# Optimization experiments

Hardware: AMD Instinct MI355X
Metric: run time of the kernel (lower is better)

The kernel has to match this reference:

```python
import jax, jax.numpy as jnp
import numpy as np

K = 64          # number of tags, incl. BOS/EOS
V = 50000       # vocab size (excl. BOS/EOS words)
D = 128         # lexicon embedding dim
BOS_T = K - 2   # BOS tag index
EOS_T = K - 1   # EOS tag index
BATCH = 8192
L = 126         # interior words per sentence (n = L + 2 incl. BOS/EOS)
EPS = 1e-45     # smoothing added to A and B in updateAB


def setup_inputs() -> dict:
    key = jax.random.key(0)
    k1, k2, k3, k4 = jax.random.split(key, 4)
    words = jax.random.randint(k1, (BATCH, L), 0, V, dtype=jnp.int32)
    ThetaB = 0.01 * jax.random.uniform(k2, (K, D), dtype=jnp.float32)
    WA = 0.01 * jax.random.uniform(k3, (K, K), dtype=jnp.float32)
    E = jax.random.normal(k4, (V, D), dtype=jnp.float32)
    return {"words": words, "ThetaB": ThetaB, "WA": WA, "E": E}


def reference(words, ThetaB, WA, E):
    # updateAB(): A = softmax(WA) with BOS column forced to prob 0 (-inf logit)
    WAm = WA.at[:, BOS_T].set(-jnp.inf)
    A = jax.nn.softmax(WAm, axis=1) + EPS                       # [K, K]
    B = jax.nn.softmax(ThetaB @ E.T, axis=1)                    # [K, V]
    B = B.at[EOS_T, :].set(0.0).at[BOS_T, :].set(0.0) + EPS
    logA = jnp.log(A)                                           # [K, K]
    logB = jnp.log(B)                                           # [K, V]

    # Emission log-probs gathered per token: [L, B, K]
    em = jnp.swapaxes(logB.T[words], 0, 1)

    # alpha_0: one-hot (in log space) at BOS tag
    alpha0 = jnp.full((words.shape[0], K), -jnp.inf, dtype=logA.dtype)
    alpha0 = alpha0.at[:, BOS_T].set(0.0)

    def step(alpha, e):
        # alpha: [B, K] over prev tags; logsumexp over prev tag axis
        new = jax.nn.logsumexp(alpha[:, :, None] + logA[None, :, :], axis=1) + e
        return new, None

    alpha, _ = jax.lax.scan(step, alpha0, em)
    # Final transition into EOS tag (no emission): log Z per sentence, [B]
    logZ = jax.nn.logsumexp(alpha + logA[None, :, EOS_T], axis=1)
    return logZ
```

## Files before the change

kernel.cpp:

```cpp
#include <hip/hip_runtime.h>
#include <hip/hip_bf16.h>
#include <math.h>


#define KT 64
#define VV 50000
#define DD 128
#define BOS_T 62
#define EOS_T 63
#define LLEN 126
#define EPSF 1e-45f
#define SCALE_F 65536.0f
#define LOG_TOTAL_SCALE (2016.0f * 0.6931471805599453f)
#define NBLK 782
#define PBLK 784
#define TPH 14
#define NPH 9

#define BTN_OFF   0
#define A_OFF     6400000
#define SUM_OFF   6416384
#define PART_OFF  6416640

typedef short short8 __attribute__((ext_vector_type(8)));
typedef float f32x4  __attribute__((ext_vector_type(4)));

union U8 { short8 v; unsigned u[4]; short s[8]; };

static __device__ inline unsigned short f2bf_u(float x) {
    __hip_bfloat16 h = __float2bfloat16(x);
    return *reinterpret_cast<unsigned short*>(&h);
}
static __device__ inline short f2bf(float x) { return (short)f2bf_u(x); }

#if __has_builtin(__builtin_amdgcn_cvt_pk_bf16_f32)
typedef __bf16 bf16x2 __attribute__((ext_vector_type(2)));
static __device__ inline unsigned pk2(float a, float b) {
    bf16x2 r = __builtin_amdgcn_cvt_pk_bf16_f32(a, b);
    return *reinterpret_cast<unsigned*>(&r);
}
#else
static __device__ inline unsigned pk2(float a, float b) {
    union { float f; unsigned u; } ua, ub;
    ua.f = a; ub.f = b;
    return ((ua.u + 0x8000u) >> 16) | ((ub.u + 0x8000u) & 0xFFFF0000u);
}
#endif
static __device__ inline float lo16(unsigned u) { union { unsigned i; float f; } c; c.i = u << 16;        return c.f; }
static __device__ inline float hi16(unsigned u) { union { unsigned i; float f; } c; c.i = u & 0xffff0000u; return c.f; }

#if __has_builtin(__builtin_amdgcn_global_load_lds)
#define GLLDS(gp, lbase)                                                        \
    __builtin_amdgcn_global_load_lds(                                           \
        (__attribute__((address_space(1))) void*)const_cast<unsigned short*>(gp),\
        (__attribute__((address_space(3))) void*)(lbase), 16, 0, 0)
#else
#define GLLDS(gp, lbase)                                                        \
    do { *(uint4*)((unsigned short*)(lbase) + (threadIdx.x & 63) * 8) =         \
             *(const uint4*)(gp); } while (0)
#endif

__global__ __launch_bounds__(256) void k_emit(const float* __restrict__ ThetaB,
                                              const float* __restrict__ E,
                                              unsigned short* __restrict__ btn_bf,
                                              float* __restrict__ partial) {
    __shared__ float red[4][KT];
    int t    = threadIdx.x;
    int lane = t & 63;
    int w    = t >> 6;
    int n    = lane & 15;
    int q    = lane >> 4;
    int v0   = (blockIdx.x * 4 + w) * 16;

    int rowE = v0 + n;
    bool valid = rowE < VV;
    rowE = valid ? rowE : VV - 1;
    float4 ex[4][2];
#pragma unroll
    for (int kt = 0; kt < 4; ++kt) {
        const float* p = E + (size_t)rowE * DD + kt * 32 + q * 8;
        ex[kt][0] = *(const float4*)p;
        ex[kt][1] = *(const float4*)(p + 4);
    }

    short8 Th[4][4];
#pragma unroll
    for (int kt = 0; kt < 4; ++kt)
#pragma unroll
        for (int mt = 0; mt < 4; ++mt) {
            const float* p = ThetaB + (mt * 16 + n) * DD + kt * 32 + q * 8;
            float4 x = *(const float4*)p;
            float4 y = *(const float4*)(p + 4);
            U8 f;
            f.u[0] = pk2(x.x, x.y); f.u[1] = pk2(x.z, x.w);
            f.u[2] = pk2(y.x, y.y); f.u[3] = pk2(y.z, y.w);
            Th[kt][mt] = f.v;
        }

    short8 Ef[4];
#pragma unroll
    for (int kt = 0; kt < 4; ++kt) {
        U8 f;
        f.u[0] = pk2(ex[kt][0].x, ex[kt][0].y); f.u[1] = pk2(ex[kt][0].z, ex[kt][0].w);
        f.u[2] = pk2(ex[kt][1].x, ex[kt][1].y); f.u[3] = pk2(ex[kt][1].z, ex[kt][1].w);
        Ef[kt] = f.v;
    }

#pragma unroll
    for (int mt = 0; mt < 4; ++mt) {
        f32x4 C = {0.f, 0.f, 0.f, 0.f};
#pragma unroll
        for (int kt = 0; kt < 4; ++kt)
            C = __builtin_amdgcn_mfma_f32_16x16x32_bf16(Th[kt][mt], Ef[kt], C, 0, 0, 0);
        float e[4];
#pragma unroll
        for (int r = 0; r < 4; ++r) e[r] = __expf(C[r]);
        if (valid) {
            uint2 st = make_uint2(pk2(e[0], e[1]), pk2(e[2], e[3]));
            *(uint2*)(btn_bf + (size_t)rowE * KT + mt * 16 + q * 4) = st;
        }
#pragma unroll
        for (int r = 0; r < 4; ++r) {
            float s = valid ? e[r] : 0.0f;
            s += __shfl_xor(s, 1, 64);
            s += __shfl_xor(s, 2, 64);
            s += __shfl_xor(s, 4, 64);
            s += __shfl_xor(s, 8, 64);
            if (n == 0) red[w][mt * 16 + q * 4 + r] = s;
        }
    }
    __syncthreads();
    if (w == 0) {
        float s = red[0][lane] + red[1][lane] + red[2][lane] + red[3][lane];
        partial[lane * PBLK + blockIdx.x] = s;
    }
}

__global__ __launch_bounds__(256) void k_sumA(const float* __restrict__ partial,
                                              const float* __restrict__ WA,
                                              float* __restrict__ sumexp,
                                              float* __restrict__ A) {
    __shared__ float r[4];
    int k = blockIdx.x;
    int t = threadIdx.x;
    float s = 0.0f;
    for (int i = t; i < NBLK; i += 256) s += partial[k * PBLK + i];
#pragma unroll
    for (int off = 32; off > 0; off >>= 1) s += __shfl_xor(s, off, 64);
    if ((t & 63) == 0) r[t >> 6] = s;
    __syncthreads();
    if (t == 0) sumexp[k] = r[0] + r[1] + r[2] + r[3];
    if (t < 64) {
        float wv = WA[k * KT + t];
        float e = (t == BOS_T) ? 0.0f : __expf(wv);
        float se = e;
#pragma unroll
        for (int off = 32; off > 0; off >>= 1) se += __shfl_xor(se, off, 64);
        A[k * KT + t] = e / se + EPSF;
    }
}

__global__ __launch_bounds__(256) void k_fwd(const int* __restrict__ words,
                                             const unsigned short* __restrict__ btn_bf,
                                             const float* __restrict__ A,
                                             const float* __restrict__ sumexp,
                                             float* __restrict__ out) {
    __shared__ int shw[16 * LLEN];
    __shared__ __attribute__((aligned(16))) unsigned short shE[2][TPH * 1024];
    int lane = threadIdx.x & 63;
    int w    = threadIdx.x >> 6;
    int n    = lane & 15;
    int qA   = lane >> 4;
    int b0   = blockIdx.x * 16;

    {
        const uint4* src = (const uint4*)(words + (size_t)b0 * LLEN);
        uint4* dst = (uint4*)shw;
        for (int idx = threadIdx.x; idx < (16 * LLEN) / 4; idx += 256)
            dst[idx] = src[idx];
    }

    short8 Af[2][4];
    short8 B0, B1;
    if (w == 3) {
#pragma unroll
        for (int mt = 0; mt < 4; ++mt) {
            int tagn = 32 * (mt >> 1) + 8 * (n >> 2) + 4 * (mt & 1) + (n & 3);
            float s = sumexp[tagn];
            float rsn = (tagn == BOS_T || tagn == EOS_T) ? 0.0f : (SCALE_F / s);
#pragma unroll
            for (int kt = 0; kt < 2; ++kt) {
                U8 f;
#pragma unroll
                for (int j = 0; j < 8; ++j)
                    f.s[j] = f2bf(A[(kt * 32 + qA * 8 + j) * KT + tagn] * rsn);
                Af[kt][mt] = f.v;
            }
        }
        U8 z; z.u[0] = z.u[1] = z.u[2] = z.u[3] = 0;
        B0 = z.v;
        U8 o; o.u[0] = o.u[1] = o.u[2] = o.u[3] = 0;
        if (qA == 3) o.s[6] = (short)0x3F80;
        B1 = o.v;
    }
    __syncthreads();

#define PSTAGE(bb, p_)                                                        \
    do {                                                                      \
        for (int s_ = w; s_ < TPH; s_ += 3) {                                 \
            int wd_ = shw[n * LLEN + (p_) * TPH + s_];                        \
            const unsigned short* g_ = btn_bf + (size_t)wd_ * KT + qA * 8;    \
            GLLDS(g_, &shE[bb][s_ * 1024]);                                   \
            GLLDS(g_ + 32, &shE[bb][s_ * 1024 + 512]);                        \
        }                                                                     \
        asm volatile("s_waitcnt vmcnt(0)" ::: "memory");                      \
    } while (0)

#define LDE(bb, ss, hh) (*(const uint4*)(&shE[bb][(ss) * 1024 + (hh) * 512] + lane * 8))

    if (w < 3) PSTAGE(0, 0);
    __syncthreads();

    for (int p = 0; p < NPH; ++p) {
        int b = p & 1;
        if (w < 3) {
            if (p + 1 < NPH) PSTAGE((p + 1) & 1, p + 1);
        } else {
            uint4 a0 = LDE(b, 0, 0), a1 = LDE(b, 0, 1);
            uint4 c0 = LDE(b, 1, 0), c1 = LDE(b, 1, 1);
#pragma unroll
            for (int s = 0; s < TPH; ++s) {
                uint4 e0 = a0, e1 = a1;
                a0 = c0; a1 = c1;
                int s2 = (s + 2 < TPH) ? s + 2 : TPH - 1;
                c0 = LDE(b, s2, 0); c1 = LDE(b, s2, 1);

                f32x4 C[4];
#pragma unroll
                for (int mt = 0; mt < 4; ++mt) {
                    f32x4 acc = {0.f, 0.f, 0.f, 0.f};
                    acc = __builtin_amdgcn_mfma_f32_16x16x32_bf16(Af[0][mt], B0, acc, 0, 0, 0);
                    acc = __builtin_amdgcn_mfma_f32_16x16x32_bf16(Af[1][mt], B1, acc, 0, 0, 0);
                    C[mt] = acc;
                }
                U8 f0, f1;
                f0.u[0] = pk2(C[0][0] * lo16(e0.x), C[0][1] * hi16(e0.x));
                f0.u[1] = pk2(C[0][2] * lo16(e0.y), C[0][3] * hi16(e0.y));
                f0.u[2] = pk2(C[1][0] * lo16(e0.z), C[1][1] * hi16(e0.z));
                f0.u[3] = pk2(C[1][2] * lo16(e0.w), C[1][3] * hi16(e0.w));
                f1.u[0] = pk2(C[2][0] * lo16(e1.x), C[2][1] * hi16(e1.x));
                f1.u[1] = pk2(C[2][2] * lo16(e1.y), C[2][3] * hi16(e1.y));
                f1.u[2] = pk2(C[3][0] * lo16(e1.z), C[3][1] * hi16(e1.z));
                f1.u[3] = pk2(C[3][2] * lo16(e1.w), C[3][3] * hi16(e1.w));
                B0 = f0.v; B1 = f1.v;
            }
        }
        __syncthreads();
    }

    if (w == 3) {
        short8 Afin[2];
#pragma unroll
        for (int kt = 0; kt < 2; ++kt) {
            U8 f;
#pragma unroll
            for (int j = 0; j < 8; ++j)
                f.s[j] = (n == 0) ? f2bf(A[(kt * 32 + qA * 8 + j) * KT + EOS_T]) : (short)0;
            Afin[kt] = f.v;
        }
        f32x4 Cf = {0.f, 0.f, 0.f, 0.f};
        Cf = __builtin_amdgcn_mfma_f32_16x16x32_bf16(Afin[0], B0, Cf, 0, 0, 0);
        Cf = __builtin_amdgcn_mfma_f32_16x16x32_bf16(Afin[1], B1, Cf, 0, 0, 0);
        if (qA == 0)
            out[b0 + n] = logf(Cf[0]) - LOG_TOTAL_SCALE;
    }
}

extern "C" void kernel_launch(void* const* d_in, const int* in_sizes, int n_in,
                              void* d_out, int out_size, void* d_ws, size_t ws_size,
                              hipStream_t stream) {
    const int*   words  = (const int*)d_in[0];
    const float* ThetaB = (const float*)d_in[1];
    const float* WA     = (const float*)d_in[2];
    const float* E      = (const float*)d_in[3];
    float* out = (float*)d_out;

    char* ws = (char*)d_ws;
    unsigned short* btn_bf = (unsigned short*)(ws + BTN_OFF);
    float* A       = (float*)(ws + A_OFF);
    float* sumexp  = (float*)(ws + SUM_OFF);
    float* partial = (float*)(ws + PART_OFF);

    k_emit<<<NBLK, 256, 0, stream>>>(ThetaB, E, btn_bf, partial);
    k_sumA<<<KT, 256, 0, stream>>>(partial, WA, sumexp, A);
    k_fwd<<<8192 / 16, 256, 0, stream>>>(words, btn_bf, A, sumexp, out);
}
```

Before: 129.8 us.

## Store emission table in FP8 and restage forward pass with larger phases

```diff
diff --git a/kernel.cpp b/kernel.cpp
--- a/kernel.cpp
+++ b/kernel.cpp
@@ -14,16 +14,17 @@
 #define LOG_TOTAL_SCALE (2016.0f * 0.6931471805599453f)
 #define NBLK 782
 #define PBLK 784
-#define TPH 14
-#define NPH 9
+#define TPH 21
+#define NPH 6
 
 #define BTN_OFF   0
-#define A_OFF     6400000
-#define SUM_OFF   6416384
-#define PART_OFF  6416640
+#define A_OFF     3200000
+#define SUM_OFF   3216384
+#define PART_OFF  3216640
 
 typedef short short8 __attribute__((ext_vector_type(8)));
 typedef float f32x4  __attribute__((ext_vector_type(4)));
+typedef float f32x2  __attribute__((ext_vector_type(2)));
 
 union U8 { short8 v; unsigned u[4]; short s[8]; };
 
@@ -49,20 +50,51 @@
 static __device__ inline float lo16(unsigned u) { union { unsigned i; float f; } c; c.i = u << 16;        return c.f; }
 static __device__ inline float hi16(unsigned u) { union { unsigned i; float f; } c; c.i = u & 0xffff0000u; return c.f; }
 
+#if __has_builtin(__builtin_amdgcn_cvt_pk_fp8_f32)
+static __device__ inline unsigned pk4f8(float a, float b, float c, float d) {
+    int v = __builtin_amdgcn_cvt_pk_fp8_f32(a, b, 0, false);
+    v = __builtin_amdgcn_cvt_pk_fp8_f32(c, d, v, true);
+    return (unsigned)v;
+}
+#else
+static __device__ inline unsigned enc1f8(float x) {
+    union { float f; unsigned u; } c; c.f = x;
+    unsigned u = c.u & 0x7FFFFFFFu;
+    unsigned r = u + 0x7FFFFu + ((u >> 20) & 1u);
+    return ((r >> 20) - (120u << 3)) & 0x7Fu;
+}
+static __device__ inline unsigned pk4f8(float a, float b, float c, float d) {
+    return enc1f8(a) | (enc1f8(b) << 8) | (enc1f8(c) << 16) | (enc1f8(d) << 24);
+}
+#endif
+
+#if __has_builtin(__builtin_amdgcn_cvt_pk_f32_fp8)
+static __device__ inline f32x2 dec2lo(unsigned w) { return __builtin_amdgcn_cvt_pk_f32_fp8((int)w, false); }
+static __device__ inline f32x2 dec2hi(unsigned w) { return __builtin_amdgcn_cvt_pk_f32_fp8((int)w, true); }
+#else
+static __device__ inline float dec1f8(unsigned b) {
+    union { unsigned u; float f; } c;
+    c.u = ((b & 0x80u) << 24) | (((b & 0x7Fu) << 20) + (120u << 23));
+    return c.f;
+}
+static __device__ inline f32x2 dec2lo(unsigned w) { f32x2 r; r.x = dec1f8(w & 0xFF); r.y = dec1f8((w >> 8) & 0xFF); return r; }
+static __device__ inline f32x2 dec2hi(unsigned w) { f32x2 r; r.x = dec1f8((w >> 16) & 0xFF); r.y = dec1f8(w >> 24); return r; }
+#endif
+
 #if __has_builtin(__builtin_amdgcn_global_load_lds)
 #define GLLDS(gp, lbase)                                                        \
     __builtin_amdgcn_global_load_lds(                                           \
-        (__attribute__((address_space(1))) void*)const_cast<unsigned short*>(gp),\
+        (__attribute__((address_space(1))) void*)const_cast<unsigned char*>(gp),\
         (__attribute__((address_space(3))) void*)(lbase), 16, 0, 0)
 #else
 #define GLLDS(gp, lbase)                                                        \
-    do { *(uint4*)((unsigned short*)(lbase) + (threadIdx.x & 63) * 8) =         \
+    do { *(uint4*)((unsigned char*)(lbase) + (threadIdx.x & 63) * 16) =         \
              *(const uint4*)(gp); } while (0)
 #endif
 
 __global__ __launch_bounds__(256) void k_emit(const float* __restrict__ ThetaB,
                                               const float* __restrict__ E,
-                                              unsigned short* __restrict__ btn_bf,
+                                              unsigned char* __restrict__ btn8,
                                               float* __restrict__ partial) {
     __shared__ float red[4][KT];
     int t    = threadIdx.x;
@@ -116,8 +148,8 @@
 #pragma unroll
         for (int r = 0; r < 4; ++r) e[r] = __expf(C[r]);
         if (valid) {
-            uint2 st = make_uint2(pk2(e[0], e[1]), pk2(e[2], e[3]));
-            *(uint2*)(btn_bf + (size_t)rowE * KT + mt * 16 + q * 4) = st;
+            int pos = 16 * ((2 * mt + (q >> 1)) & 3) + 8 * (mt >> 1) + (q & 1) * 4;
+            *(unsigned*)(btn8 + (size_t)rowE * KT + pos) = pk4f8(e[0], e[1], e[2], e[3]);
         }
 #pragma unroll
         for (int r = 0; r < 4; ++r) {
@@ -161,12 +193,12 @@
 }
 
 __global__ __launch_bounds__(256) void k_fwd(const int* __restrict__ words,
-                                             const unsigned short* __restrict__ btn_bf,
+                                             const unsigned char* __restrict__ btn8,
                                              const float* __restrict__ A,
                                              const float* __restrict__ sumexp,
                                              float* __restrict__ out) {
     __shared__ int shw[16 * LLEN];
-    __shared__ __attribute__((aligned(16))) unsigned short shE[2][TPH * 1024];
+    __shared__ __attribute__((aligned(16))) unsigned char shE[2][TPH * 1024];
     int lane = threadIdx.x & 63;
     int w    = threadIdx.x >> 6;
     int n    = lane & 15;
@@ -209,14 +241,13 @@
     do {                                                                      \
         for (int s_ = w; s_ < TPH; s_ += 3) {                                 \
             int wd_ = shw[n * LLEN + (p_) * TPH + s_];                        \
-            const unsigned short* g_ = btn_bf + (size_t)wd_ * KT + qA * 8;    \
+            const unsigned char* g_ = btn8 + (size_t)wd_ * KT + qA * 16;      \
             GLLDS(g_, &shE[bb][s_ * 1024]);                                   \
-            GLLDS(g_ + 32, &shE[bb][s_ * 1024 + 512]);                        \
         }                                                                     \
         asm volatile("s_waitcnt vmcnt(0)" ::: "memory");                      \
     } while (0)
 
-#define LDE(bb, ss, hh) (*(const uint4*)(&shE[bb][(ss) * 1024 + (hh) * 512] + lane * 8))
+#define LDE(bb, ss) (*(const uint4*)(&shE[bb][(ss) * 1024] + lane * 16))
 
     if (w < 3) PSTAGE(0, 0);
     __syncthreads();
@@ -226,14 +257,19 @@
         if (w < 3) {
             if (p + 1 < NPH) PSTAGE((p + 1) & 1, p + 1);
         } else {
-            uint4 a0 = LDE(b, 0, 0), a1 = LDE(b, 0, 1);
-            uint4 c0 = LDE(b, 1, 0), c1 = LDE(b, 1, 1);
+            uint4 r0 = LDE(b, 0);
+            uint4 r1 = LDE(b, 1);
 #pragma unroll
             for (int s = 0; s < TPH; ++s) {
-                uint4 e0 = a0, e1 = a1;
-                a0 = c0; a1 = c1;
+                uint4 rc = r0;
+                r0 = r1;
                 int s2 = (s + 2 < TPH) ? s + 2 : TPH - 1;
-                c0 = LDE(b, s2, 0); c1 = LDE(b, s2, 1);
+                r1 = LDE(b, s2);
+
+                f32x2 d0 = dec2lo(rc.x), d1 = dec2hi(rc.x);
+                f32x2 d2 = dec2lo(rc.y), d3 = dec2hi(rc.y);
+                f32x2 d4 = dec2lo(rc.z), d5 = dec2hi(rc.z);
+                f32x2 d6 = dec2lo(rc.w), d7 = dec2hi(rc.w);
 
                 f32x4 C[4];
 #pragma unroll
@@ -244,14 +280,14 @@
                     C[mt] = acc;
                 }
                 U8 f0, f1;
-                f0.u[0] = pk2(C[0][0] * lo16(e0.x), C[0][1] * hi16(e0.x));
-                f0.u[1] = pk2(C[0][2] * lo16(e0.y), C[0][3] * hi16(e0.y));
-                f0.u[2] = pk2(C[1][0] * lo16(e0.z), C[1][1] * hi16(e0.z));
-                f0.u[3] = pk2(C[1][2] * lo16(e0.w), C[1][3] * hi16(e0.w));
-                f1.u[0] = pk2(C[2][0] * lo16(e1.x), C[2][1] * hi16(e1.x));
-                f1.u[1] = pk2(C[2][2] * lo16(e1.y), C[2][3] * hi16(e1.y));
-                f1.u[2] = pk2(C[3][0] * lo16(e1.z), C[3][1] * hi16(e1.z));
-                f1.u[3] = pk2(C[3][2] * lo16(e1.w), C[3][3] * hi16(e1.w));
+                f0.u[0] = pk2(C[0][0] * d0.x, C[0][1] * d0.y);
+                f0.u[1] = pk2(C[0][2] * d1.x, C[0][3] * d1.y);
+                f0.u[2] = pk2(C[1][0] * d2.x, C[1][1] * d2.y);
+                f0.u[3] = pk2(C[1][2] * d3.x, C[1][3] * d3.y);
+                f1.u[0] = pk2(C[2][0] * d4.x, C[2][1] * d4.y);
+                f1.u[1] = pk2(C[2][2] * d5.x, C[2][3] * d5.y);
+                f1.u[2] = pk2(C[3][0] * d6.x, C[3][1] * d6.y);
+                f1.u[3] = pk2(C[3][2] * d7.x, C[3][3] * d7.y);
                 B0 = f0.v; B1 = f1.v;
             }
         }
@@ -286,12 +322,12 @@
     float* out = (float*)d_out;
 
     char* ws = (char*)d_ws;
-    unsigned short* btn_bf = (unsigned short*)(ws + BTN_OFF);
+    unsigned char* btn8 = (unsigned char*)(ws + BTN_OFF);
     float* A       = (float*)(ws + A_OFF);
     float* sumexp  = (float*)(ws + SUM_OFF);
     float* partial = (float*)(ws + PART_OFF);
 
-    k_emit<<<NBLK, 256, 0, stream>>>(ThetaB, E, btn_bf, partial);
+    k_emit<<<NBLK, 256, 0, stream>>>(ThetaB, E, btn8, partial);
     k_sumA<<<KT, 256, 0, stream>>>(partial, WA, sumexp, A);
-    k_fwd<<<8192 / 16, 256, 0, stream>>>(words, btn_bf, A, sumexp, out);
-}
+    k_fwd<<<8192 / 16, 256, 0, stream>>>(words, btn8, A, sumexp, out);
+}
```

After: 127.7 us. No clear change (-1.6%).
